# Kernel tuning notes

Hardware: AMD Instinct MI355X
Metric: run time of the kernel (lower is better)

Reference implementation:

```python
import jax, jax.numpy as jnp
import numpy as np

TEMP = 0.07
HARD_K = 512
EMB_D = 768
PROJ_D = 128
QUEUE = 32768
BATCH = 2048
NUM_CLASSES = 2


def setup_inputs() -> dict:
    key = jax.random.key(0)
    ks = jax.random.split(key, 8)
    embeddings = jax.random.normal(ks[0], (BATCH, EMB_D), dtype=jnp.float32)
    labels = jax.random.randint(ks[1], (BATCH,), 0, NUM_CLASSES)
    # projector params: Linear(D,D) -> ReLU -> Linear(D,128)
    W1 = jax.random.normal(ks[2], (EMB_D, EMB_D), dtype=jnp.float32) * 0.02
    b1 = jnp.zeros((EMB_D,), dtype=jnp.float32)
    W2 = jax.random.normal(ks[3], (EMB_D, PROJ_D), dtype=jnp.float32) * 0.02
    b2 = jnp.zeros((PROJ_D,), dtype=jnp.float32)
    # queue buffers: L2-normalized random embeddings (as in __init__) with valid labels
    qe = jax.random.normal(ks[4], (QUEUE, PROJ_D), dtype=jnp.float32)
    queue_embeddings = qe / jnp.linalg.norm(qe, axis=1, keepdims=True)
    queue_labels = jax.random.randint(ks[5], (QUEUE,), 0, NUM_CLASSES)
    return {
        'embeddings': embeddings, 'labels': labels,
        'W1': W1, 'b1': b1, 'W2': W2, 'b2': b2,
        'queue_embeddings': queue_embeddings, 'queue_labels': queue_labels,
    }


def reference(embeddings, labels, W1, b1, W2, b2, queue_embeddings, queue_labels):
    n = embeddings.shape[0]
    # projector + L2 normalize
    h = jax.nn.relu(embeddings @ W1 + b1)
    z = h @ W2 + b2
    z = z / jnp.linalg.norm(z, axis=1, keepdims=True)  # (N, 128)

    # pairwise in-batch similarities, scaled by temperature
    S = (z @ z.T) / TEMP  # (N, N)
    same = labels[:, None] == labels[None, :]
    eye = jnp.eye(n, dtype=bool)
    pos_mask = same & ~eye           # positives: same label, not self
    neg_mask = ~same                 # in-batch negatives: different label

    # logsumexp over in-batch negatives per anchor (-inf rows -> -inf, handled by logaddexp)
    neg_batch = jnp.where(neg_mask, S, -jnp.inf)
    lse_batch = jax.scipy.special.logsumexp(neg_batch, axis=1)  # (N,)

    # hard negatives from queue: opposite-label, top-K by similarity
    sims_q = z @ queue_embeddings.T  # (N, Q)
    opp = (queue_labels[None, :] != labels[:, None]) & (queue_labels[None, :] >= 0)
    masked_q = jnp.where(opp, sims_q, -jnp.inf)
    topk_vals, _ = jax.lax.top_k(masked_q, HARD_K)  # (N, K); -inf pads drop from logsumexp
    # fallback (no opposite-label entries): first K queue embeddings regardless of label
    fallback = sims_q[:, :HARD_K]
    has_opp = opp.any(axis=1, keepdims=True)
    neg_q = jnp.where(has_opp, topk_vals, fallback) / TEMP
    lse_queue = jax.scipy.special.logsumexp(neg_q, axis=1)  # (N,)

    # all negatives for anchor i: batch negatives ++ queue hard negatives
    lse_neg = jnp.logaddexp(lse_batch, lse_queue)  # (N,)

    # per positive pair (i, j): log_prob = pos_sim - logsumexp([pos_sim, negs])
    log_prob = S - jnp.logaddexp(S, lse_neg[:, None])  # (N, N)
    losses = jnp.where(pos_mask, -log_prob, 0.0)
    count = pos_mask.sum()
    return jnp.where(count > 0, losses.sum() / count.astype(losses.dtype), 0.0)
```

## Files before the change

kernel.cpp:

```cpp
#include <hip/hip_runtime.h>
#include <hip/hip_fp16.h>

#define BATCH_N   2048
#define EMB_D_    768
#define PROJ_D_   128
#define QUEUE_N   32768
#define HARD_K_   512
static constexpr float INV_T  = 1.0f / 0.07f;
static constexpr float WLO    = 0.12f;
static constexpr float S8ENC  = 255.0f / 0.88f;
static constexpr float BINW   = 0.88f / 255.0f;

typedef __attribute__((ext_vector_type(8))) short short8;
typedef __attribute__((ext_vector_type(4))) short short4v;
typedef __attribute__((ext_vector_type(4))) float f32x4;

__device__ __forceinline__ unsigned short f2bf(float f) {
    unsigned u = __float_as_uint(f);
    unsigned r = u + 0x7fffu + ((u >> 16) & 1u);
    return (unsigned short)(r >> 16);
}
__device__ __forceinline__ float bf2f(short s) {
    return __uint_as_float(((unsigned)(unsigned short)s) << 16);
}
__device__ __forceinline__ int opp_of(int mylab, const int* __restrict__ qcnt) {
    const int same = (mylab == 0) ? qcnt[0] : ((mylab == 1) ? qcnt[1] : 0);
    return qcnt[2] - same;
}

__global__ void __launch_bounds__(256) prep(const float* __restrict__ emb, short* __restrict__ embb,
                                            const float* __restrict__ queue, short* __restrict__ qb,
                                            const int* __restrict__ qlab, int* __restrict__ qpart,
                                            const float* __restrict__ W1, short* __restrict__ w1t,
                                            const float* __restrict__ W2, short* __restrict__ w2t,
                                            const int* __restrict__ labels, int* __restrict__ rcnt,
                                            int* __restrict__ pc) {
    __shared__ float tile[64][65];
    const int b = blockIdx.x, t = threadIdx.x;
    if (b < 1536) {
        const int i = b * 256 + t;
        const float4 f = ((const float4*)emb)[i];
        short4v o = {(short)f2bf(f.x), (short)f2bf(f.y), (short)f2bf(f.z), (short)f2bf(f.w)};
        ((short4v*)embb)[i] = o;
    } else if (b < 5632) {
        const int i = (b - 1536) * 256 + t;
        const float4 f = ((const float4*)queue)[i];
        short4v o = {(short)f2bf(f.x), (short)f2bf(f.y), (short)f2bf(f.z), (short)f2bf(f.w)};
        ((short4v*)qb)[i] = o;
    } else if (b < 5664) {
        const int i = (b - 5632) * 256 + t;
        int c0 = 0, c1 = 0, cv = 0;
        for (int j = i; j < QUEUE_N; j += 8192) {
            const int q = qlab[j];
            c0 += (q == 0); c1 += (q == 1); cv += (q >= 0);
        }
        #pragma unroll
        for (int o = 32; o > 0; o >>= 1) {
            c0 += __shfl_xor(c0, o); c1 += __shfl_xor(c1, o); cv += __shfl_xor(cv, o);
        }
        int* red = (int*)tile;
        const int wv = t >> 6;
        if ((t & 63) == 0) { red[wv * 4 + 0] = c0; red[wv * 4 + 1] = c1; red[wv * 4 + 2] = cv; }
        __syncthreads();
        if (t == 0) {
            const int bb = (b - 5632) * 4;
            qpart[bb + 0] = red[0] + red[4] + red[8]  + red[12];
            qpart[bb + 1] = red[1] + red[5] + red[9]  + red[13];
            qpart[bb + 2] = red[2] + red[6] + red[10] + red[14];
        }
    } else if (b < 5832) {
        const int bid = b - 5664;
        const float* A; short* At; int R, C, bx, by;
        if (bid < 144) { A = W1; At = w1t; R = EMB_D_; C = EMB_D_;  bx = (bid % 12) * 64; by = (bid / 12) * 64; }
        else { const int b2 = bid - 144; A = W2; At = w2t; R = EMB_D_; C = PROJ_D_; bx = (b2 & 1) * 64; by = (b2 >> 1) * 64; }
        const int tc = t & 63, tg = t >> 6;
        #pragma unroll
        for (int i = 0; i < 16; i++) {
            const int r = tg * 16 + i;
            tile[r][tc] = A[(size_t)(by + r) * C + bx + tc];
        }
        __syncthreads();
        #pragma unroll
        for (int i = 0; i < 16; i++) {
            const int r = tg * 16 + i;
            At[(size_t)(bx + r) * R + by + tc] = (short)f2bf(tile[tc][r]);
        }
    } else {
        int c = 0;
        for (int j = t; j < BATCH_N; j += 256) c += (labels[j] == 0);
        #pragma unroll
        for (int o = 32; o > 0; o >>= 1) c += __shfl_xor(c, o);
        int* red = (int*)tile;
        if ((t & 63) == 0) red[t >> 6] = c;
        __syncthreads();
        if (t == 0) rcnt[0] = red[0] + red[1] + red[2] + red[3];
        if (t < 8) pc[t] = 0;
    }
}

__global__ void __launch_bounds__(256) mfma_h64(const short* __restrict__ Ab,
                                                const short* __restrict__ Bb,
                                                const float* __restrict__ bias,
                                                short* __restrict__ C,
                                                int N, int K) {
    __shared__ __align__(16) short As[64 * 128];
    __shared__ __align__(16) short Bs[128 * 128];
    const int t = threadIdx.x;
    const int lane = t & 63, wv = t >> 6;
    const int l16 = lane & 15, l4 = lane >> 4;
    const int m0 = blockIdx.y * 64, n0 = blockIdx.x * 128;
    const int wn = wv * 32;

    f32x4 acc[4][2];
    #pragma unroll
    for (int i = 0; i < 4; ++i)
        #pragma unroll
        for (int j = 0; j < 2; ++j) acc[i][j] = f32x4{0.f, 0.f, 0.f, 0.f};

    for (int kb = 0; kb < K; kb += 128) {
        __syncthreads();
        #pragma unroll
        for (int it = 0; it < 4; ++it) {
            const int r = it * 4 + wv, row = r * 4 + l4, cg = l16 ^ (row & 15);
            __builtin_amdgcn_global_load_lds(
                (const __attribute__((address_space(1))) void*)(Ab + (size_t)(m0 + row) * K + kb + cg * 8),
                (__attribute__((address_space(3))) void*)(As + r * 512), 16, 0, 0);
        }
        #pragma unroll
        for (int it = 0; it < 8; ++it) {
            const int r = it * 4 + wv, row = r * 4 + l4, cg = l16 ^ (row & 15);
            __builtin_amdgcn_global_load_lds(
                (const __attribute__((address_space(1))) void*)(Bb + (size_t)(n0 + row) * K + kb + cg * 8),
                (__attribute__((address_space(3))) void*)(Bs + r * 512), 16, 0, 0);
        }
        __syncthreads();
        #pragma unroll
        for (int ks = 0; ks < 4; ++ks) {
            short8 af[4], bfr[2];
            const int ch = (ks * 4 + l4) ^ l16;
            #pragma unroll
            for (int i = 0; i < 4; ++i)
                af[i] = *(const short8*)(As + (i * 16 + l16) * 128 + ch * 8);
            #pragma unroll
            for (int j = 0; j < 2; ++j)
                bfr[j] = *(const short8*)(Bs + (wn + j * 16 + l16) * 128 + ch * 8);
            #pragma unroll
            for (int i = 0; i < 4; ++i)
                #pragma unroll
                for (int j = 0; j < 2; ++j)
                    acc[i][j] = __builtin_amdgcn_mfma_f32_16x16x32_bf16(af[i], bfr[j], acc[i][j], 0, 0, 0);
        }
    }

    float bsv[2];
    #pragma unroll
    for (int j = 0; j < 2; ++j) bsv[j] = bias[n0 + wn + j * 16 + l16];
    #pragma unroll
    for (int i = 0; i < 4; ++i)
        #pragma unroll
        for (int r = 0; r < 4; ++r) {
            const int m = m0 + i * 16 + l4 * 4 + r;
            #pragma unroll
            for (int j = 0; j < 2; ++j) {
                const int n = n0 + wn + j * 16 + l16;
                const float v = fmaxf(acc[i][j][r] + bsv[j], 0.0f);
                C[(size_t)m * N + n] = (short)f2bf(v);
            }
        }
}

__global__ void __launch_bounds__(256) znorm_perm(const short* __restrict__ Ab,
                                                  const short* __restrict__ Bb,
                                                  const float* __restrict__ bias,
                                                  short* __restrict__ zb,
                                                  const int* __restrict__ qlab,
                                                  const int* __restrict__ labels,
                                                  const int* __restrict__ qpart,
                                                  const int* __restrict__ rcnt,
                                                  int* __restrict__ qcnt,
                                                  int* __restrict__ colidx,
                                                  int* __restrict__ qlabp,
                                                  int* __restrict__ rowmap,
                                                  int* __restrict__ rlabp,
                                                  int* __restrict__ pc) {
    __shared__ __align__(16) short As[32 * 128];
    __shared__ __align__(16) short Bs[128 * 128];
    __shared__ float ssq[32];
    __shared__ int wcnt[4][3];
    __shared__ int gbase[3];
    const int blk = blockIdx.x;
    const int t = threadIdx.x;
    const int lane = t & 63, wv = t >> 6;

    if (blk >= 64) {
        const unsigned long long below = (1ull << lane) - 1ull;
        int q0 = 0, q1 = 0, qv = 0;
        for (int i = 0; i < 32; ++i) {
            q0 += qpart[i * 4]; q1 += qpart[i * 4 + 1]; qv += qpart[i * 4 + 2];
        }
        if (blk < 192) {
            const int cb = blk - 64;
            if (cb == 0 && t == 0) { qcnt[0] = q0; qcnt[1] = q1; qcnt[2] = qv; }
            const int j = cb * 256 + t;
            const int q = qlab[j];
            const int cls = (q == 0) ? 0 : ((q == 1) ? 1 : 2);
            const unsigned long long b0 = __ballot(cls == 0);
            const unsigned long long b1 = __ballot(cls == 1);
            const unsigned long long b2 = __ballot(cls == 2);
            const int rank = (cls == 0) ? __popcll(b0 & below)
                           : ((cls == 1) ? __popcll(b1 & below) : __popcll(b2 & below));
            if (lane == 0) {
                wcnt[wv][0] = __popcll(b0); wcnt[wv][1] = __popcll(b1); wcnt[wv][2] = __popcll(b2);
            }
            __syncthreads();
            if (t < 3) {
                const int tot = wcnt[0][t] + wcnt[1][t] + wcnt[2][t] + wcnt[3][t];
                gbase[t] = atomicAdd(&pc[t], tot);
            }
            __syncthreads();
            int wb = 0;
            #pragma unroll
            for (int w = 0; w < 4; ++w) if (w < wv) wb += wcnt[w][cls];
            const int cbase = (cls == 0) ? 0 : ((cls == 1) ? q0 : q0 + q1);
            const int pos = cbase + gbase[cls] + wb + rank;
            colidx[pos] = j; qlabp[pos] = q;
        } else {
            const int r = (blk - 192) * 256 + t;
            const int l = labels[r];
            const int cls = (l == 0) ? 0 : 1;
            const unsigned long long b0 = __ballot(cls == 0);
            const unsigned long long b1 = __ballot(cls == 1);
            const int rank = (cls == 0) ? __popcll(b0 & below) : __popcll(b1 & below);
            if (lane == 0) { wcnt[wv][0] = __popcll(b0); wcnt[wv][1] = __popcll(b1); }
            __syncthreads();
            if (t < 2) {
                const int tot = wcnt[0][t] + wcnt[1][t] + wcnt[2][t] + wcnt[3][t];
                gbase[t] = atomicAdd(&pc[3 + t], tot);
            }
            __syncthreads();
            int wb = 0;
            #pragma unroll
            for (int w = 0; w < 4; ++w) if (w < wv) wb += wcnt[w][cls];
            const int cbase = (cls == 0) ? 0 : rcnt[0];
            const int pos = cbase + gbase[cls] + wb + rank;
            rowmap[pos] = r; rlabp[pos] = l;
        }
        return;
    }

    const int l16 = lane & 15, l4 = lane >> 4;
    const int m0 = blk * 32;
    const int wn = wv * 32;
    const int K = EMB_D_;

    if (t < 32) ssq[t] = 0.0f;

    f32x4 acc[2][2];
    #pragma unroll
    for (int i = 0; i < 2; ++i)
        #pragma unroll
        for (int j = 0; j < 2; ++j) acc[i][j] = f32x4{0.f, 0.f, 0.f, 0.f};

    for (int kb = 0; kb < K; kb += 128) {
        __syncthreads();
        #pragma unroll
        for (int it = 0; it < 2; ++it) {
            const int r = it * 4 + wv, row = r * 4 + l4, cg = l16 ^ (row & 15);
            __builtin_amdgcn_global_load_lds(
                (const __attribute__((address_space(1))) void*)(Ab + (size_t)(m0 + row) * K + kb + cg * 8),
                (__attribute__((address_space(3))) void*)(As + r * 512), 16, 0, 0);
        }
        #pragma unroll
        for (int it = 0; it < 8; ++it) {
            const int r = it * 4 + wv, row = r * 4 + l4, cg = l16 ^ (row & 15);
            __builtin_amdgcn_global_load_lds(
                (const __attribute__((address_space(1))) void*)(Bb + (size_t)(row) * K + kb + cg * 8),
                (__attribute__((address_space(3))) void*)(Bs + r * 512), 16, 0, 0);
        }
        __syncthreads();
        #pragma unroll
        for (int ks = 0; ks < 4; ++ks) {
            short8 af[2], bfr[2];
            const int ch = (ks * 4 + l4) ^ l16;
            #pragma unroll
            for (int i = 0; i < 2; ++i)
                af[i] = *(const short8*)(As + (i * 16 + l16) * 128 + ch * 8);
            #pragma unroll
            for (int j = 0; j < 2; ++j)
                bfr[j] = *(const short8*)(Bs + (wn + j * 16 + l16) * 128 + ch * 8);
            #pragma unroll
            for (int i = 0; i < 2; ++i)
                #pragma unroll
                for (int j = 0; j < 2; ++j)
                    acc[i][j] = __builtin_amdgcn_mfma_f32_16x16x32_bf16(af[i], bfr[j], acc[i][j], 0, 0, 0);
        }
    }

    float bsv[2];
    #pragma unroll
    for (int j = 0; j < 2; ++j) bsv[j] = bias[wn + j * 16 + l16];
    #pragma unroll
    for (int i = 0; i < 2; ++i)
        #pragma unroll
        for (int r = 0; r < 4; ++r) {
            float p = 0.0f;
            #pragma unroll
            for (int j = 0; j < 2; ++j) {
                acc[i][j][r] += bsv[j];
                p += acc[i][j][r] * acc[i][j][r];
            }
            #pragma unroll
            for (int o = 8; o > 0; o >>= 1) p += __shfl_xor(p, o);
            if (l16 == 0) atomicAdd(&ssq[i * 16 + l4 * 4 + r], p);
        }
    __syncthreads();
    #pragma unroll
    for (int i = 0; i < 2; ++i)
        #pragma unroll
        for (int r = 0; r < 4; ++r) {
            const int lrow = i * 16 + l4 * 4 + r;
            const float inv = rsqrtf(ssq[lrow]);
            #pragma unroll
            for (int j = 0; j < 2; ++j)
                zb[(size_t)(m0 + lrow) * PROJ_D_ + wn + j * 16 + l16] =
                    (short)f2bf(acc[i][j][r] * inv);
        }
}

__global__ void __launch_bounds__(256) mfma_mask8(const short* __restrict__ Ab,
                                                  const short* __restrict__ Bb,
                                                  unsigned char* __restrict__ codes,
                                                  const int* __restrict__ rlabp,
                                                  const int* __restrict__ qlabp,
                                                  const int* __restrict__ colidx,
                                                  const int* __restrict__ rowmap,
                                                  const int* __restrict__ qcnt,
                                                  const int* __restrict__ rcnt) {
    const int m0 = blockIdx.y * 128;
    const int c0 = qcnt[0], c1v = qcnt[1], r0 = rcnt[0];
    int lo, hi;
    if (m0 + 128 <= r0)      { lo = c0; hi = c0 + c1v; }
    else if (m0 >= r0)       { lo = 0;  hi = c0; }
    else                     { lo = 0;  hi = c0 + c1v; }
    const int bs = blockIdx.x * 512;
    if (bs + 512 <= lo || bs >= hi) return;

    __shared__ __align__(16) short As[128 * 128];
    __shared__ __align__(16) short Bs[128 * 128];
    const int t = threadIdx.x;
    const int lane = t & 63, wv = t >> 6;
    const int l16 = lane & 15, l4 = lane >> 4;
    const int wm = (wv & 1) * 64, wn = (wv >> 1) * 64;

    int ra[8], ca[32], la[16], qa[16];
    #pragma unroll
    for (int it = 0; it < 8; ++it)
        ra[it] = rowmap[m0 + (it * 4 + wv) * 4 + l4];
    #pragma unroll
    for (int tt = 0; tt < 4; ++tt)
        #pragma unroll
        for (int it = 0; it < 8; ++it)
            ca[tt * 8 + it] = colidx[bs + tt * 128 + (it * 4 + wv) * 4 + l4];
    #pragma unroll
    for (int i = 0; i < 4; ++i)
        #pragma unroll
        for (int r = 0; r < 4; ++r)
            la[i * 4 + r] = rlabp[m0 + wm + i * 16 + l4 * 4 + r];
    #pragma unroll
    for (int tt = 0; tt < 4; ++tt)
        #pragma unroll
        for (int j = 0; j < 4; ++j)
            qa[tt * 4 + j] = qlabp[bs + tt * 128 + wn + j * 16 + l16];

    #pragma unroll
    for (int it = 0; it < 8; ++it) {
        const int r = it * 4 + wv, row = r * 4 + l4, cg = l16 ^ (row & 15);
        __builtin_amdgcn_global_load_lds(
            (const __attribute__((address_space(1))) void*)(Ab + (size_t)ra[it] * 128 + cg * 8),
            (__attribute__((address_space(3))) void*)(As + r * 512), 16, 0, 0);
    }
    #pragma unroll
    for (int it = 0; it < 8; ++it) {
        const int r = it * 4 + wv, row = r * 4 + l4, cg = l16 ^ (row & 15);
        __builtin_amdgcn_global_load_lds(
            (const __attribute__((address_space(1))) void*)(Bb + (size_t)ca[it] * 128 + cg * 8),
            (__attribute__((address_space(3))) void*)(Bs + r * 512), 16, 0, 0);
    }
    const float C0 = 1.0f - WLO * S8ENC;
    __syncthreads();

    #pragma unroll
    for (int tt = 0; tt < 4; ++tt) {
        const int n0 = bs + tt * 128;

        f32x4 acc[4][4];
        #pragma unroll
        for (int i = 0; i < 4; ++i)
            #pragma unroll
            for (int j = 0; j < 4; ++j) acc[i][j] = f32x4{0.f, 0.f, 0.f, 0.f};

        #pragma unroll
        for (int ks = 0; ks < 4; ++ks) {
            short8 af[4], bfr[4];
            const int ch = (ks * 4 + l4) ^ l16;
            #pragma unroll
            for (int i = 0; i < 4; ++i) {
                af[i]  = *(const short8*)(As + (wm + i * 16 + l16) * 128 + ch * 8);
                bfr[i] = *(const short8*)(Bs + (wn + i * 16 + l16) * 128 + ch * 8);
            }
            #pragma unroll
            for (int i = 0; i < 4; ++i)
                #pragma unroll
                for (int j = 0; j < 4; ++j)
                    acc[i][j] = __builtin_amdgcn_mfma_f32_16x16x32_bf16(af[i], bfr[j], acc[i][j], 0, 0, 0);
        }

        if (tt < 3) {
            __syncthreads();
            #pragma unroll
            for (int it = 0; it < 8; ++it) {
                const int r = it * 4 + wv, row = r * 4 + l4, cg = l16 ^ (row & 15);
                __builtin_amdgcn_global_load_lds(
                    (const __attribute__((address_space(1))) void*)(Bb + (size_t)ca[(tt + 1) * 8 + it] * 128 + cg * 8),
                    (__attribute__((address_space(3))) void*)(Bs + r * 512), 16, 0, 0);
            }
        }

        float a0[4], a1[4];
        #pragma unroll
        for (int j = 0; j < 4; ++j) {
            const int q = qa[tt * 4 + j];
            a0[j] = (q >= 0 && q != 0) ? C0 : -1e9f;
            a1[j] = (q >= 0 && q != 1) ? C0 : -1e9f;
        }
        #pragma unroll
        for (int i = 0; i < 4; ++i) {
            #pragma unroll
            for (int r = 0; r < 4; ++r) {
                const int m  = m0 + wm + i * 16 + l4 * 4 + r;
                const bool z = (la[i * 4 + r] == 0);
                unsigned pk = 0;
                #pragma unroll
                for (int j = 0; j < 4; ++j) {
                    const float add = z ? a0[j] : a1[j];
                    const float f = fmaf(acc[i][j][r], S8ENC, add);
#if __has_builtin(__builtin_amdgcn_cvt_pk_u8_f32)
                    pk = __builtin_amdgcn_cvt_pk_u8_f32(f, j, pk);
#else
                    const unsigned c = (unsigned)fminf(fmaxf(f, 0.0f), 255.0f);
                    pk |= c << (8 * j);
#endif
                }
                *(unsigned*)(codes + (size_t)m * QUEUE_N + n0 + wn + l16 * 4) = pk;
            }
        }
        if (tt < 3) __syncthreads();
    }
}

__device__ __forceinline__ void find_crossing(int* hist, int* grp, int target,
                                              int* s_bin, int* s_chi) {
    const int t = threadIdx.x;
    const int b0 = hist[4*t], b1 = hist[4*t+1], b2 = hist[4*t+2], b3 = hist[4*t+3];
    grp[t] = b0 + b1 + b2 + b3;
    __syncthreads();
    for (int off = 1; off < 256; off <<= 1) {
        int add = (t + off < 256) ? grp[t + off] : 0;
        __syncthreads();
        grp[t] += add;
        __syncthreads();
    }
    int cab = (t < 255) ? grp[t + 1] : 0;
    const int hb[4] = {b0, b1, b2, b3};
    #pragma unroll
    for (int i = 3; i >= 0; i--) {
        const int h = hb[i];
        if (cab < target && cab + h >= target) { *s_bin = 4*t + i; *s_chi = cab; }
        cab += h;
    }
    __syncthreads();
}

#define FOR_ALL_VALS(BODY)                                                   \
    _Pragma("unroll")                                                        \
    for (int _k = 0; _k < 64; _k++) {                                        \
        const float2 _f = __half22float2(*(const __half2*)&dv[_k]);          \
        { const float v = _f.x; BODY }                                       \
        { const float v = _f.y; BODY }                                       \
    }

__global__ void __launch_bounds__(256) tail_fused(const unsigned char* __restrict__ codes,
                                                  const int* __restrict__ qcnt,
                                                  const int* __restrict__ rlabp,
                                                  const int* __restrict__ rowmap,
                                                  const short* __restrict__ zb,
                                                  const short* __restrict__ qb,
                                                  const int* __restrict__ qlab,
                                                  float* __restrict__ lseq,
                                                  short* __restrict__ Sbuf) {
    __shared__ __align__(16) short As[128 * 128];
    __shared__ __align__(16) short Bs[128 * 128];
    __shared__ int s_bin, s_chi, s_bin2, s_chi2;
    __shared__ float scf[4];
    __shared__ int sci[4];
    const int bid = blockIdx.x, t = threadIdx.x;

    if (bid >= BATCH_N) {
        const int q = bid - BATCH_N;
        const int lane = t & 63, wv = t >> 6;
        const int l16 = lane & 15, l4 = lane >> 4;
        const int m0 = (q >> 4) * 128, n0 = (q & 15) * 128;

        #pragma unroll
        for (int it = 0; it < 8; ++it) {
            const int r = it * 4 + wv, row = r * 4 + l4, cg = l16 ^ (row & 15);
            __builtin_amdgcn_global_load_lds(
                (const __attribute__((address_space(1))) void*)(zb + (size_t)(m0 + row) * 128 + cg * 8),
                (__attribute__((address_space(3))) void*)(As + r * 512), 16, 0, 0);
        }
        #pragma unroll
        for (int it = 0; it < 8; ++it) {
            const int r = it * 4 + wv, row = r * 4 + l4, cg = l16 ^ (row & 15);
            __builtin_amdgcn_global_load_lds(
                (const __attribute__((address_space(1))) void*)(zb + (size_t)(n0 + row) * 128 + cg * 8),
                (__attribute__((address_space(3))) void*)(Bs + r * 512), 16, 0, 0);
        }
        __syncthreads();

        const int wm = (wv & 1) * 64, wn = (wv >> 1) * 64;
        f32x4 acc[4][4];
        #pragma unroll
        for (int i = 0; i < 4; ++i)
            #pragma unroll
            for (int j = 0; j < 4; ++j) acc[i][j] = f32x4{0.f, 0.f, 0.f, 0.f};

        #pragma unroll
        for (int ks = 0; ks < 4; ++ks) {
            short8 af[4], bfr[4];
            const int ch = (ks * 4 + l4) ^ l16;
            #pragma unroll
            for (int i = 0; i < 4; ++i) {
                af[i]  = *(const short8*)(As + (wm + i * 16 + l16) * 128 + ch * 8);
                bfr[i] = *(const short8*)(Bs + (wn + i * 16 + l16) * 128 + ch * 8);
            }
            #pragma unroll
            for (int i = 0; i < 4; ++i)
                #pragma unroll
                for (int j = 0; j < 4; ++j)
                    acc[i][j] = __builtin_amdgcn_mfma_f32_16x16x32_bf16(af[i], bfr[j], acc[i][j], 0, 0, 0);
        }
        #pragma unroll
        for (int i = 0; i < 4; ++i)
            #pragma unroll
            for (int r = 0; r < 4; ++r) {
                const int m = m0 + wm + i * 16 + l4 * 4 + r;
                union { unsigned short u[4]; uint2 d; } pk;
                #pragma unroll
                for (int j = 0; j < 4; ++j) pk.u[j] = f2bf(acc[i][j][r]);
                *(uint2*)(Sbuf + (size_t)m * BATCH_N + n0 + wn + l16 * 4) = pk.d;
            }
        return;
    }

    const int p = bid;
    const int orig  = rowmap[p];
    const int myLab = rlabp[p];
    const int opp   = opp_of(myLab, qcnt);
    bool fb = (opp < HARD_K_);
    if (!fb) {
        int* hist = (int*)Bs;
        int* suf  = (int*)(Bs + 512);
        hist[t] = 0;
        __syncthreads();

        const int c0 = qcnt[0];
        const int lo = (myLab == 0) ? c0 : 0;
        const int hi = (myLab == 0) ? c0 + qcnt[1] : c0;
        const int klo = (lo & ~511) >> 4;
        const int khi = ((hi + 511) & ~511) >> 4;

        const uint4* rowp = (const uint4*)(codes + (size_t)p * QUEUE_N);
        for (int k = klo + t; k < khi; k += 256) {
            const uint4 u = rowp[k];
            const unsigned w[4] = {u.x, u.y, u.z, u.w};
            #pragma unroll
            for (int q = 0; q < 4; q++)
                #pragma unroll
                for (int s = 0; s < 4; s++) {
                    const int c = (w[q] >> (8 * s)) & 0xFF;
                    if (c) atomicAdd(&hist[c], 1);
                }
        }
        __syncthreads();

        suf[t] = hist[t];
        __syncthreads();
        for (int off = 1; off < 256; off <<= 1) {
            int add = (t + off < 256) ? suf[t + off] : 0;
            __syncthreads();
            suf[t] += add;
            __syncthreads();
        }
        const int total = suf[1];
        if (total >= HARD_K_) {
            {
                const int above = (t < 255) ? suf[t + 1] : 0;
                if (suf[t] >= HARD_K_ && above < HARD_K_) s_bin = t;
            }
            __syncthreads();
            const int b = s_bin;

            float e = 0.0f;
            if (t > b && hist[t]) e = (float)hist[t] * __expf((WLO + ((float)t - 0.5f) * BINW - 1.0f) * INV_T);
            #pragma unroll
            for (int o = 32; o > 0; o >>= 1) e += __shfl_xor(e, o);
            if ((t & 63) == 0) scf[t >> 6] = e;
            __syncthreads();
            if (t == 0) {
                const float Eab  = scf[0] + scf[1] + scf[2] + scf[3];
                const int   cab  = (b < 255) ? suf[b + 1] : 0;
                const float ebin = __expf((WLO + ((float)b - 0.5f) * BINW - 1.0f) * INV_T);
                const float sadj = Eab + (float)(HARD_K_ - cab) * ebin;
                lseq[orig] = INV_T + __logf(sadj);
            }
            return;
        }
        __syncthreads();
    }

    float* zrow = (float*)As;
    int*   fh   = (int*)(As + 512);
    int*   grp  = (int*)(As + 2560);
    if (t < 128) zrow[t] = bf2f(zb[(size_t)orig * 128 + t]);
    __syncthreads();

    const int mylab = myLab;
    unsigned dv[64];
    float rm = -1e30f, rs = 0.0f;
    for (int k = 0; k < 128; k++) {
        const int j = t + 256 * k;
        float d = 0.0f;
        #pragma unroll
        for (int c = 0; c < 16; ++c) {
            const short8 qv = *(const short8*)(qb + (size_t)j * 128 + c * 8);
            #pragma unroll
            for (int e = 0; e < 8; ++e) d += zrow[c * 8 + e] * bf2f(qv[e]);
        }
        if (j < HARD_K_) {
            const float sv = d * INV_T;
            if (sv > rm) { rs = rs * __expf(rm - sv) + 1.0f; rm = sv; }
            else         { rs += __expf(sv - rm); }
        }
        const int q = qlab[j];
        const float mv = (q != mylab && q >= 0) ? d : -65504.0f;
        const __half h = __float2half(mv);
        unsigned short* pp = (unsigned short*)&dv[k >> 1];
        pp[k & 1] = *(const unsigned short*)&h;
    }

    if (opp == 0) {
        #pragma unroll
        for (int o = 32; o > 0; o >>= 1) {
            const float om = __shfl_xor(rm, o), os = __shfl_xor(rs, o);
            const float nm = fmaxf(rm, om);
            rs = rs * __expf(rm - nm) + os * __expf(om - nm);
            rm = nm;
        }
        if ((t & 63) == 0) { scf[t >> 6] = rm; ((float*)sci)[t >> 6] = rs; }
        __syncthreads();
        if (t == 0) {
            float M = -1e30f, Sx = 0.0f;
            for (int w = 0; w < 4; w++) {
                const float nm = fmaxf(M, scf[w]);
                Sx = Sx * __expf(M - nm) + ((float*)sci)[w] * __expf(scf[w] - nm);
                M = nm;
            }
            lseq[orig] = M + __logf(Sx);
        }
        return;
    }
    if (opp < HARD_K_) {
        float mm = -1e30f, ss = 0.0f;
        FOR_ALL_VALS(
            if (v > -60000.0f) {
                const float sv = v * INV_T;
                if (sv > mm) { ss = ss * __expf(mm - sv) + 1.0f; mm = sv; }
                else         { ss += __expf(sv - mm); }
            } )
        #pragma unroll
        for (int o = 32; o > 0; o >>= 1) {
            const float om = __shfl_xor(mm, o), os = __shfl_xor(ss, o);
            const float nm = fmaxf(mm, om);
            ss = ss * __expf(mm - nm) + os * __expf(om - nm);
            mm = nm;
        }
        if ((t & 63) == 0) { scf[t >> 6] = mm; ((float*)sci)[t >> 6] = ss; }
        __syncthreads();
        if (t == 0) {
            float M = -1e30f, Sx = 0.0f;
            for (int w = 0; w < 4; w++) {
                const float nm = fmaxf(M, scf[w]);
                Sx = Sx * __expf(M - nm) + ((float*)sci)[w] * __expf(scf[w] - nm);
                M = nm;
            }
            lseq[orig] = M + __logf(Sx);
        }
        return;
    }

    float mloc = -1e30f;
    FOR_ALL_VALS( mloc = fmaxf(mloc, v); )
    #pragma unroll
    for (int o = 32; o > 0; o >>= 1) mloc = fmaxf(mloc, __shfl_xor(mloc, o));
    if ((t & 63) == 0) scf[t >> 6] = mloc;
    __syncthreads();
    const float m = fmaxf(fmaxf(scf[0], scf[1]), fmaxf(scf[2], scf[3]));

    int c1 = 0, c2 = 0;
    const float w1 = m - 0.25f, w2 = m - 1.0f;
    FOR_ALL_VALS( c1 += (v >= w1); c2 += (v >= w2); )
    #pragma unroll
    for (int o = 32; o > 0; o >>= 1) { c1 += __shfl_xor(c1, o); c2 += __shfl_xor(c2, o); }
    if ((t & 63) == 0) { sci[t >> 6] = c1; }
    __syncthreads();
    const int C1 = sci[0] + sci[1] + sci[2] + sci[3];
    __syncthreads();
    if ((t & 63) == 0) { sci[t >> 6] = c2; }
    __syncthreads();
    const int C2 = sci[0] + sci[1] + sci[2] + sci[3];

    float lo;
    if      (C1 >= HARD_K_) lo = w1;
    else if (C2 >= HARD_K_) lo = w2;
    else                    lo = -1.01f;
    const float range = m - lo;
    const float scale = 1024.0f / range;

    for (int k = t; k < 1024; k += 256) fh[k] = 0;
    __syncthreads();
    FOR_ALL_VALS(
        if (v >= lo) {
            const float bf = fminf((v - lo) * scale, 1023.0f);
            atomicAdd(&fh[(int)bf], 1);
        } )
    __syncthreads();
    find_crossing(fh, grp, HARD_K_, &s_bin, &s_chi);
    const int   bin1 = s_bin, chi1 = s_chi;
    const float binw = range * (1.0f / 1024.0f);
    const float lo1  = lo + bin1 * binw;
    const float ssc  = 1024.0f / binw;

    for (int k = t; k < 1024; k += 256) fh[k] = 0;
    __syncthreads();
    FOR_ALL_VALS(
        if (v >= lo) {
            const float bf = fminf((v - lo) * scale, 1023.0f);
            if ((int)bf == bin1) {
                const float sf = fminf(fmaxf((v - lo1) * ssc, 0.0f), 1023.0f);
                atomicAdd(&fh[(int)sf], 1);
            }
        } )
    __syncthreads();
    find_crossing(fh, grp, HARD_K_ - chi1, &s_bin2, &s_chi2);
    const float thr = lo1 + s_bin2 * (binw * (1.0f / 1024.0f));

    float sl = 0.0f; int cg = 0;
    FOR_ALL_VALS( if (v > thr) { cg++; sl += __expf((v - m) * INV_T); } )
    #pragma unroll
    for (int o = 32; o > 0; o >>= 1) { sl += __shfl_xor(sl, o); cg += __shfl_xor(cg, o); }
    if ((t & 63) == 0) { scf[t >> 6] = sl; sci[t >> 6] = cg; }
    __syncthreads();
    if (t == 0) {
        const float slt = scf[0] + scf[1] + scf[2] + scf[3];
        const int   cgt = sci[0] + sci[1] + sci[2] + sci[3];
        const float sadj = slt + ((float)HARD_K_ - (float)cgt) * __expf((thr - m) * INV_T);
        lseq[orig] = m * INV_T + __logf(sadj);
    }
}

__global__ void __launch_bounds__(256) batch_row_loss(const short* __restrict__ S,
                                                      const int* __restrict__ labels,
                                                      const float* __restrict__ lse_queue,
                                                      float* __restrict__ part_out,
                                                      int* __restrict__ cnt_out) {
    const int t = threadIdx.x;
    const int wv = t >> 6, lane = t & 63;
    const int row = blockIdx.x * 4 + wv;
    __shared__ int plab[BATCH_N];
    for (int idx = t; idx < BATCH_N; idx += 256) {
        const int col = (idx & ~63) + ((idx & 3) << 4) + ((idx >> 2) & 15);
        plab[idx] = labels[col];
    }
    __syncthreads();
    const int myLab = labels[row];
    const uint4* rp = (const uint4*)(S + (size_t)row * BATCH_N);

    float v[32]; int lb[32];
    #pragma unroll
    for (int kk = 0; kk < 4; kk++) {
        const uint4 u = rp[lane + 64 * kk];
        const unsigned w[4] = {u.x, u.y, u.z, u.w};
        const int base = (lane + 64 * kk) * 8;
        #pragma unroll
        for (int q = 0; q < 4; q++) {
            v[kk * 8 + 2 * q]     = __uint_as_float(w[q] << 16);
            v[kk * 8 + 2 * q + 1] = __uint_as_float(w[q] & 0xFFFF0000u);
            lb[kk * 8 + 2 * q]     = plab[base + 2 * q];
            lb[kk * 8 + 2 * q + 1] = plab[base + 2 * q + 1];
        }
    }

    const float REF = INV_T;
    float sneg = 0.0f;
    #pragma unroll
    for (int k = 0; k < 32; k++) {
        const float ev = __expf(v[k] * INV_T - REF);
        sneg += (lb[k] != myLab) ? ev : 0.0f;
    }
    #pragma unroll
    for (int o = 32; o > 0; o >>= 1) sneg += __shfl_xor(sneg, o);
    const float lseb = (sneg > 0.0f) ? REF + __logf(sneg) : -1e30f;
    const float Lq = lse_queue[row];
    const float mx0 = fmaxf(lseb, Lq), mn0 = fminf(lseb, Lq);
    const float L = mx0 + __logf(1.0f + __expf(mn0 - mx0));

    float part = 0.0f; int cnt = 0;
    #pragma unroll
    for (int k = 0; k < 32; k++) {
        const int idx = ((lane + 64 * (k >> 3)) * 8) + (k & 7);
        const int col = (idx & ~63) + ((idx & 3) << 4) + ((idx >> 2) & 15);
        if (lb[k] == myLab && col != row) {
            const float sv = v[k] * INV_T;
            const float mx = fmaxf(sv, L), mn = fminf(sv, L);
            part += (mx - sv) + __logf(1.0f + __expf(mn - mx));
            cnt++;
        }
    }
    #pragma unroll
    for (int o = 32; o > 0; o >>= 1) { part += __shfl_xor(part, o); cnt += __shfl_xor(cnt, o); }
    if (lane == 0) { part_out[row] = part; cnt_out[row] = cnt; }
}

__global__ void __launch_bounds__(256) finalize_loss(const float* __restrict__ part,
                                                     const int* __restrict__ cnt,
                                                     float* __restrict__ out) {
    const int t = threadIdx.x;
    float s = 0.0f; int c = 0;
    #pragma unroll
    for (int k = 0; k < 8; k++) { s += part[t + 256 * k]; c += cnt[t + 256 * k]; }
    #pragma unroll
    for (int o = 32; o > 0; o >>= 1) { s += __shfl_xor(s, o); c += __shfl_xor(c, o); }
    __shared__ float sf[4]; __shared__ int sc[4];
    if ((t & 63) == 0) { sf[t >> 6] = s; sc[t >> 6] = c; }
    __syncthreads();
    if (t == 0) {
        const float st = sf[0] + sf[1] + sf[2] + sf[3];
        const int   ct = sc[0] + sc[1] + sc[2] + sc[3];
        out[0] = (ct > 0) ? (st / (float)ct) : 0.0f;
    }
}

extern "C" void kernel_launch(void* const* d_in, const int* in_sizes, int n_in,
                              void* d_out, int out_size, void* d_ws, size_t ws_size,
                              hipStream_t stream) {
    const float* emb    = (const float*)d_in[0];
    const int*   labels = (const int*)  d_in[1];
    const float* W1     = (const float*)d_in[2];
    const float* b1     = (const float*)d_in[3];
    const float* W2     = (const float*)d_in[4];
    const float* b2     = (const float*)d_in[5];
    const float* queue  = (const float*)d_in[6];
    const int*   qlab   = (const int*)  d_in[7];

    char* ws = (char*)d_ws;
    short*         Sbuf  = (short*)        (ws);
    unsigned char* codes = (unsigned char*)(ws + 16777216);
    short*         embb  = (short*)        (ws + 83886080);
    short*         hbf   = (short*)        (ws + 87031808);
    short*         zb    = (short*)        (ws + 90177536);
    short*         qb    = (short*)        (ws + 90701824);
    short*         w1t   = (short*)        (ws + 99090432);
    short*         w2t   = (short*)        (ws + 100270080);
    float*         lseq  = (float*)        (ws + 100466688);
    int*           qcnt  = (int*)          (ws + 100474880);
    int*           rcnt  = (int*)          (ws + 100474944);
    int*           pc    = (int*)          (ws + 100475008);
    int*           qpart = (int*)          (ws + 100475072);
    float*         partb = (float*)        (ws + 100475584);
    int*           cntb  = (int*)          (ws + 100483776);
    int*           colidx= (int*)          (ws + 100491968);
    int*           qlabp = (int*)          (ws + 100623040);
    int*           rowmap= (int*)          (ws + 100754112);
    int*           rlabp = (int*)          (ws + 100762304);

    dim3 blk(256);
    prep<<<dim3(5833), blk, 0, stream>>>(emb, embb, queue, qb, qlab, qpart, W1, w1t, W2, w2t, labels, rcnt, pc);
    mfma_h64<<<dim3(EMB_D_ / 128, BATCH_N / 64), blk, 0, stream>>>(embb, w1t, b1, hbf, EMB_D_, EMB_D_);
    znorm_perm<<<dim3(200), blk, 0, stream>>>(hbf, w2t, b2, zb, qlab, labels, qpart, rcnt,
                                              qcnt, colidx, qlabp, rowmap, rlabp, pc);
    mfma_mask8<<<dim3(QUEUE_N / 512, BATCH_N / 128), blk, 0, stream>>>(zb, qb, codes, rlabp, qlabp, colidx, rowmap, qcnt, rcnt);
    tail_fused<<<dim3(BATCH_N + 256), blk, 0, stream>>>(codes, qcnt, rlabp, rowmap, zb, qb, qlab, lseq, Sbuf);
    batch_row_loss<<<dim3(BATCH_N / 4), blk, 0, stream>>>(Sbuf, labels, lseq, partb, cntb);
    finalize_loss<<<1, blk, 0, stream>>>(partb, cntb, (float*)d_out);
}
```

Baseline: 192.6 us.

## Rebalance tiles, move S GEMM into mask kernel, fuse finalize, privatize histograms

The batch S=z·zᵀ GEMM moves out of the top-k tail kernel into the queue mask/GEMM kernel as extra blocks. Both GEMMs now use 64-row tiles, which doubles block count and cuts LDS use. The top-k kernel gets a smaller, dedicated LDS footprint with per-wave privatized histograms to reduce atomic contention. The finalize reduction is fused into the row-loss kernel with a last-block-done counter, dropping one launch. This adds risk: the done counter at pc+6 must be zeroed on every call, and the code shown does not make that visible.

```diff
diff --git a/kernel.cpp b/kernel.cpp
--- a/kernel.cpp
+++ b/kernel.cpp
@@ -327,34 +327,90 @@
         }
 }
 
-__global__ void __launch_bounds__(256) mfma_mask8(const short* __restrict__ Ab,
-                                                  const short* __restrict__ Bb,
-                                                  unsigned char* __restrict__ codes,
-                                                  const int* __restrict__ rlabp,
-                                                  const int* __restrict__ qlabp,
-                                                  const int* __restrict__ colidx,
-                                                  const int* __restrict__ rowmap,
-                                                  const int* __restrict__ qcnt,
-                                                  const int* __restrict__ rcnt) {
-    const int m0 = blockIdx.y * 128;
+__global__ void __launch_bounds__(256) mask8_spack(const short* __restrict__ zb,
+                                                   const short* __restrict__ qb,
+                                                   unsigned char* __restrict__ codes,
+                                                   const int* __restrict__ rlabp,
+                                                   const int* __restrict__ qlabp,
+                                                   const int* __restrict__ colidx,
+                                                   const int* __restrict__ rowmap,
+                                                   const int* __restrict__ qcnt,
+                                                   const int* __restrict__ rcnt,
+                                                   short* __restrict__ Sbuf) {
+    __shared__ __align__(16) short As[64 * 128];
+    __shared__ __align__(16) short Bs[128 * 128];
+    const int bid = blockIdx.x, t = threadIdx.x;
+    const int lane = t & 63, wv = t >> 6;
+    const int l16 = lane & 15, l4 = lane >> 4;
+    const int wm = (wv & 1) * 32, wn = (wv >> 1) * 64;
+
+    if (bid >= 2048) {
+        const int q = bid - 2048;
+        const int m0 = (q >> 4) * 64, n0 = (q & 15) * 128;
+        #pragma unroll
+        for (int it = 0; it < 4; ++it) {
+            const int r = it * 4 + wv, row = r * 4 + l4, cg = l16 ^ (row & 15);
+            __builtin_amdgcn_global_load_lds(
+                (const __attribute__((address_space(1))) void*)(zb + (size_t)(m0 + row) * 128 + cg * 8),
+                (__attribute__((address_space(3))) void*)(As + r * 512), 16, 0, 0);
+        }
+        #pragma unroll
+        for (int it = 0; it < 8; ++it) {
+            const int r = it * 4 + wv, row = r * 4 + l4, cg = l16 ^ (row & 15);
+            __builtin_amdgcn_global_load_lds(
+                (const __attribute__((address_space(1))) void*)(zb + (size_t)(n0 + row) * 128 + cg * 8),
+                (__attribute__((address_space(3))) void*)(Bs + r * 512), 16, 0, 0);
+        }
+        __syncthreads();
+
+        f32x4 acc[2][4];
+        #pragma unroll
+        for (int i = 0; i < 2; ++i)
+            #pragma unroll
+            for (int j = 0; j < 4; ++j) acc[i][j] = f32x4{0.f, 0.f, 0.f, 0.f};
+
+        #pragma unroll
+        for (int ks = 0; ks < 4; ++ks) {
+            short8 af[2], bfr[4];
+            const int ch = (ks * 4 + l4) ^ l16;
+            #pragma unroll
+            for (int i = 0; i < 2; ++i)
+                af[i]  = *(const short8*)(As + (wm + i * 16 + l16) * 128 + ch * 8);
+            #pragma unroll
+            for (int j = 0; j < 4; ++j)
+                bfr[j] = *(const short8*)(Bs + (wn + j * 16 + l16) * 128 + ch * 8);
+            #pragma unroll
+            for (int i = 0; i < 2; ++i)
+                #pragma unroll
+                for (int j = 0; j < 4; ++j)
+                    acc[i][j] = __builtin_amdgcn_mfma_f32_16x16x32_bf16(af[i], bfr[j], acc[i][j], 0, 0, 0);
+        }
+        #pragma unroll
+        for (int i = 0; i < 2; ++i)
+            #pragma unroll
+            for (int r = 0; r < 4; ++r) {
+                const int m = m0 + wm + i * 16 + l4 * 4 + r;
+                union { unsigned short u[4]; uint2 d; } pk;
+                #pragma unroll
+                for (int j = 0; j < 4; ++j) pk.u[j] = f2bf(acc[i][j][r]);
+                *(uint2*)(Sbuf + (size_t)m * BATCH_N + n0 + wn + l16 * 4) = pk.d;
+            }
+        return;
+    }
+
+    const int bx = bid & 63, by = bid >> 6;
+    const int m0 = by * 64;
     const int c0 = qcnt[0], c1v = qcnt[1], r0 = rcnt[0];
     int lo, hi;
-    if (m0 + 128 <= r0)      { lo = c0; hi = c0 + c1v; }
-    else if (m0 >= r0)       { lo = 0;  hi = c0; }
-    else                     { lo = 0;  hi = c0 + c1v; }
-    const int bs = blockIdx.x * 512;
+    if (m0 + 64 <= r0)  { lo = c0; hi = c0 + c1v; }
+    else if (m0 >= r0)  { lo = 0;  hi = c0; }
+    else                { lo = 0;  hi = c0 + c1v; }
+    const int bs = bx * 512;
     if (bs + 512 <= lo || bs >= hi) return;
 
-    __shared__ __align__(16) short As[128 * 128];
-    __shared__ __align__(16) short Bs[128 * 128];
-    const int t = threadIdx.x;
-    const int lane = t & 63, wv = t >> 6;
-    const int l16 = lane & 15, l4 = lane >> 4;
-    const int wm = (wv & 1) * 64, wn = (wv >> 1) * 64;
-
-    int ra[8], ca[32], la[16], qa[16];
-    #pragma unroll
-    for (int it = 0; it < 8; ++it)
+    int ra[4], ca[32], la[8], qa[16];
+    #pragma unroll
+    for (int it = 0; it < 4; ++it)
         ra[it] = rowmap[m0 + (it * 4 + wv) * 4 + l4];
     #pragma unroll
     for (int tt = 0; tt < 4; ++tt)
@@ -362,7 +418,7 @@
         for (int it = 0; it < 8; ++it)
             ca[tt * 8 + it] = colidx[bs + tt * 128 + (it * 4 + wv) * 4 + l4];
     #pragma unroll
-    for (int i = 0; i < 4; ++i)
+    for (int i = 0; i < 2; ++i)
         #pragma unroll
         for (int r = 0; r < 4; ++r)
             la[i * 4 + r] = rlabp[m0 + wm + i * 16 + l4 * 4 + r];
@@ -372,18 +428,18 @@
         for (int j = 0; j < 4; ++j)
             qa[tt * 4 + j] = qlabp[bs + tt * 128 + wn + j * 16 + l16];
 
+    #pragma unroll
+    for (int it = 0; it < 4; ++it) {
+        const int r = it * 4 + wv, row = r * 4 + l4, cg = l16 ^ (row & 15);
+        __builtin_amdgcn_global_load_lds(
+            (const __attribute__((address_space(1))) void*)(zb + (size_t)ra[it] * 128 + cg * 8),
+            (__attribute__((address_space(3))) void*)(As + r * 512), 16, 0, 0);
+    }
     #pragma unroll
     for (int it = 0; it < 8; ++it) {
         const int r = it * 4 + wv, row = r * 4 + l4, cg = l16 ^ (row & 15);
         __builtin_amdgcn_global_load_lds(
-            (const __attribute__((address_space(1))) void*)(Ab + (size_t)ra[it] * 128 + cg * 8),
-            (__attribute__((address_space(3))) void*)(As + r * 512), 16, 0, 0);
-    }
-    #pragma unroll
-    for (int it = 0; it < 8; ++it) {
-        const int r = it * 4 + wv, row = r * 4 + l4, cg = l16 ^ (row & 15);
-        __builtin_amdgcn_global_load_lds(
-            (const __attribute__((address_space(1))) void*)(Bb + (size_t)ca[it] * 128 + cg * 8),
+            (const __attribute__((address_space(1))) void*)(qb + (size_t)ca[it] * 128 + cg * 8),
             (__attribute__((address_space(3))) void*)(Bs + r * 512), 16, 0, 0);
     }
     const float C0 = 1.0f - WLO * S8ENC;
@@ -393,23 +449,24 @@
     for (int tt = 0; tt < 4; ++tt) {
         const int n0 = bs + tt * 128;
 
-        f32x4 acc[4][4];
-        #pragma unroll
-        for (int i = 0; i < 4; ++i)
+        f32x4 acc[2][4];
+        #pragma unroll
+        for (int i = 0; i < 2; ++i)
             #pragma unroll
             for (int j = 0; j < 4; ++j) acc[i][j] = f32x4{0.f, 0.f, 0.f, 0.f};
 
         #pragma unroll
         for (int ks = 0; ks < 4; ++ks) {
-            short8 af[4], bfr[4];
+            short8 af[2], bfr[4];
             const int ch = (ks * 4 + l4) ^ l16;
             #pragma unroll
-            for (int i = 0; i < 4; ++i) {
+            for (int i = 0; i < 2; ++i)
                 af[i]  = *(const short8*)(As + (wm + i * 16 + l16) * 128 + ch * 8);
-                bfr[i] = *(const short8*)(Bs + (wn + i * 16 + l16) * 128 + ch * 8);
-            }
-            #pragma unroll
-            for (int i = 0; i < 4; ++i)
+            #pragma unroll
+            for (int j = 0; j < 4; ++j)
+                bfr[j] = *(const short8*)(Bs + (wn + j * 16 + l16) * 128 + ch * 8);
+            #pragma unroll
+            for (int i = 0; i < 2; ++i)
                 #pragma unroll
                 for (int j = 0; j < 4; ++j)
                     acc[i][j] = __builtin_amdgcn_mfma_f32_16x16x32_bf16(af[i], bfr[j], acc[i][j], 0, 0, 0);
@@ -421,7 +478,7 @@
             for (int it = 0; it < 8; ++it) {
                 const int r = it * 4 + wv, row = r * 4 + l4, cg = l16 ^ (row & 15);
                 __builtin_amdgcn_global_load_lds(
-                    (const __attribute__((address_space(1))) void*)(Bb + (size_t)ca[(tt + 1) * 8 + it] * 128 + cg * 8),
+                    (const __attribute__((address_space(1))) void*)(qb + (size_t)ca[(tt + 1) * 8 + it] * 128 + cg * 8),
                     (__attribute__((address_space(3))) void*)(Bs + r * 512), 16, 0, 0);
             }
         }
@@ -434,7 +491,7 @@
             a1[j] = (q >= 0 && q != 1) ? C0 : -1e9f;
         }
         #pragma unroll
-        for (int i = 0; i < 4; ++i) {
+        for (int i = 0; i < 2; ++i) {
             #pragma unroll
             for (int r = 0; r < 4; ++r) {
                 const int m  = m0 + wm + i * 16 + l4 * 4 + r;
@@ -489,88 +546,27 @@
         { const float v = _f.y; BODY }                                       \
     }
 
-__global__ void __launch_bounds__(256) tail_fused(const unsigned char* __restrict__ codes,
-                                                  const int* __restrict__ qcnt,
-                                                  const int* __restrict__ rlabp,
-                                                  const int* __restrict__ rowmap,
-                                                  const short* __restrict__ zb,
-                                                  const short* __restrict__ qb,
-                                                  const int* __restrict__ qlab,
-                                                  float* __restrict__ lseq,
-                                                  short* __restrict__ Sbuf) {
-    __shared__ __align__(16) short As[128 * 128];
-    __shared__ __align__(16) short Bs[128 * 128];
+__global__ void __launch_bounds__(256) topk_fb(const unsigned char* __restrict__ codes,
+                                               const int* __restrict__ qcnt,
+                                               const int* __restrict__ rlabp,
+                                               const int* __restrict__ rowmap,
+                                               const short* __restrict__ zb,
+                                               const short* __restrict__ qb,
+                                               const int* __restrict__ qlab,
+                                               float* __restrict__ lseq) {
+    __shared__ int hist4[1024];
+    __shared__ int grp[256];
+    __shared__ float zrow[128];
     __shared__ int s_bin, s_chi, s_bin2, s_chi2;
     __shared__ float scf[4];
     __shared__ int sci[4];
-    const int bid = blockIdx.x, t = threadIdx.x;
-
-    if (bid >= BATCH_N) {
-        const int q = bid - BATCH_N;
-        const int lane = t & 63, wv = t >> 6;
-        const int l16 = lane & 15, l4 = lane >> 4;
-        const int m0 = (q >> 4) * 128, n0 = (q & 15) * 128;
-
-        #pragma unroll
-        for (int it = 0; it < 8; ++it) {
-            const int r = it * 4 + wv, row = r * 4 + l4, cg = l16 ^ (row & 15);
-            __builtin_amdgcn_global_load_lds(
-                (const __attribute__((address_space(1))) void*)(zb + (size_t)(m0 + row) * 128 + cg * 8),
-                (__attribute__((address_space(3))) void*)(As + r * 512), 16, 0, 0);
-        }
-        #pragma unroll
-        for (int it = 0; it < 8; ++it) {
-            const int r = it * 4 + wv, row = r * 4 + l4, cg = l16 ^ (row & 15);
-            __builtin_amdgcn_global_load_lds(
-                (const __attribute__((address_space(1))) void*)(zb + (size_t)(n0 + row) * 128 + cg * 8),
-                (__attribute__((address_space(3))) void*)(Bs + r * 512), 16, 0, 0);
-        }
-        __syncthreads();
-
-        const int wm = (wv & 1) * 64, wn = (wv >> 1) * 64;
-        f32x4 acc[4][4];
-        #pragma unroll
-        for (int i = 0; i < 4; ++i)
-            #pragma unroll
-            for (int j = 0; j < 4; ++j) acc[i][j] = f32x4{0.f, 0.f, 0.f, 0.f};
-
-        #pragma unroll
-        for (int ks = 0; ks < 4; ++ks) {
-            short8 af[4], bfr[4];
-            const int ch = (ks * 4 + l4) ^ l16;
-            #pragma unroll
-            for (int i = 0; i < 4; ++i) {
-                af[i]  = *(const short8*)(As + (wm + i * 16 + l16) * 128 + ch * 8);
-                bfr[i] = *(const short8*)(Bs + (wn + i * 16 + l16) * 128 + ch * 8);
-            }
-            #pragma unroll
-            for (int i = 0; i < 4; ++i)
-                #pragma unroll
-                for (int j = 0; j < 4; ++j)
-                    acc[i][j] = __builtin_amdgcn_mfma_f32_16x16x32_bf16(af[i], bfr[j], acc[i][j], 0, 0, 0);
-        }
-        #pragma unroll
-        for (int i = 0; i < 4; ++i)
-            #pragma unroll
-            for (int r = 0; r < 4; ++r) {
-                const int m = m0 + wm + i * 16 + l4 * 4 + r;
-                union { unsigned short u[4]; uint2 d; } pk;
-                #pragma unroll
-                for (int j = 0; j < 4; ++j) pk.u[j] = f2bf(acc[i][j][r]);
-                *(uint2*)(Sbuf + (size_t)m * BATCH_N + n0 + wn + l16 * 4) = pk.d;
-            }
-        return;
-    }
-
-    const int p = bid;
+    const int p = blockIdx.x, t = threadIdx.x;
     const int orig  = rowmap[p];
     const int myLab = rlabp[p];
     const int opp   = opp_of(myLab, qcnt);
-    bool fb = (opp < HARD_K_);
-    if (!fb) {
-        int* hist = (int*)Bs;
-        int* suf  = (int*)(Bs + 512);
-        hist[t] = 0;
+
+    if (opp >= HARD_K_) {
+        for (int k = t; k < 1024; k += 256) hist4[k] = 0;
         __syncthreads();
 
         const int c0 = qcnt[0];
@@ -579,6 +575,7 @@
         const int klo = (lo & ~511) >> 4;
         const int khi = ((hi + 511) & ~511) >> 4;
 
+        int* myh = hist4 + (t >> 6) * 256;
         const uint4* rowp = (const uint4*)(codes + (size_t)p * QUEUE_N);
         for (int k = klo + t; k < khi; k += 256) {
             const uint4 u = rowp[k];
@@ -588,37 +585,37 @@
                 #pragma unroll
                 for (int s = 0; s < 4; s++) {
                     const int c = (w[q] >> (8 * s)) & 0xFF;
-                    if (c) atomicAdd(&hist[c], 1);
+                    if (c) atomicAdd(&myh[c], 1);
                 }
         }
         __syncthreads();
-
-        suf[t] = hist[t];
+        const int h = hist4[t] + hist4[256 + t] + hist4[512 + t] + hist4[768 + t];
+        grp[t] = h;
         __syncthreads();
         for (int off = 1; off < 256; off <<= 1) {
-            int add = (t + off < 256) ? suf[t + off] : 0;
+            int add = (t + off < 256) ? grp[t + off] : 0;
             __syncthreads();
-            suf[t] += add;
+            grp[t] += add;
             __syncthreads();
         }
-        const int total = suf[1];
+        const int total = grp[1];
         if (total >= HARD_K_) {
             {
-                const int above = (t < 255) ? suf[t + 1] : 0;
-                if (suf[t] >= HARD_K_ && above < HARD_K_) s_bin = t;
+                const int above = (t < 255) ? grp[t + 1] : 0;
+                if (grp[t] >= HARD_K_ && above < HARD_K_) s_bin = t;
             }
             __syncthreads();
             const int b = s_bin;
 
             float e = 0.0f;
-            if (t > b && hist[t]) e = (float)hist[t] * __expf((WLO + ((float)t - 0.5f) * BINW - 1.0f) * INV_T);
+            if (t > b && h) e = (float)h * __expf((WLO + ((float)t - 0.5f) * BINW - 1.0f) * INV_T);
             #pragma unroll
             for (int o = 32; o > 0; o >>= 1) e += __shfl_xor(e, o);
             if ((t & 63) == 0) scf[t >> 6] = e;
             __syncthreads();
             if (t == 0) {
                 const float Eab  = scf[0] + scf[1] + scf[2] + scf[3];
-                const int   cab  = (b < 255) ? suf[b + 1] : 0;
+                const int   cab  = (b < 255) ? grp[b + 1] : 0;
                 const float ebin = __expf((WLO + ((float)b - 0.5f) * BINW - 1.0f) * INV_T);
                 const float sadj = Eab + (float)(HARD_K_ - cab) * ebin;
                 lseq[orig] = INV_T + __logf(sadj);
@@ -628,9 +625,7 @@
         __syncthreads();
     }
 
-    float* zrow = (float*)As;
-    int*   fh   = (int*)(As + 512);
-    int*   grp  = (int*)(As + 2560);
+    int* fh = hist4;
     if (t < 128) zrow[t] = bf2f(zb[(size_t)orig * 128 + t]);
     __syncthreads();
 
@@ -778,15 +773,18 @@
     }
 }
 
-__global__ void __launch_bounds__(256) batch_row_loss(const short* __restrict__ S,
-                                                      const int* __restrict__ labels,
-                                                      const float* __restrict__ lse_queue,
-                                                      float* __restrict__ part_out,
-                                                      int* __restrict__ cnt_out) {
+__global__ void __launch_bounds__(256) brl_final(const short* __restrict__ S,
+                                                 const int* __restrict__ labels,
+                                                 const float* __restrict__ lse_queue,
+                                                 float* __restrict__ part_out,
+                                                 int* __restrict__ cnt_out,
+                                                 int* __restrict__ done,
+                                                 float* __restrict__ out) {
     const int t = threadIdx.x;
     const int wv = t >> 6, lane = t & 63;
     const int row = blockIdx.x * 4 + wv;
     __shared__ int plab[BATCH_N];
+    __shared__ int s_last;
     for (int idx = t; idx < BATCH_N; idx += 256) {
         const int col = (idx & ~63) + ((idx & 3) << 4) + ((idx >> 2) & 15);
         plab[idx] = labels[col];
@@ -838,16 +836,24 @@
     }
     #pragma unroll
     for (int o = 32; o > 0; o >>= 1) { part += __shfl_xor(part, o); cnt += __shfl_xor(cnt, o); }
-    if (lane == 0) { part_out[row] = part; cnt_out[row] = cnt; }
-}
-
-__global__ void __launch_bounds__(256) finalize_loss(const float* __restrict__ part,
-                                                     const int* __restrict__ cnt,
-                                                     float* __restrict__ out) {
-    const int t = threadIdx.x;
+    if (lane == 0) {
+        atomicExch(&part_out[row], part);
+        atomicExch(&cnt_out[row], cnt);
+        __threadfence();
+    }
+    __syncthreads();
+    if (t == 0) s_last = (atomicAdd(done, 1) == (int)gridDim.x - 1);
+    __syncthreads();
+    if (!s_last) return;
+
+    __threadfence();
     float s = 0.0f; int c = 0;
     #pragma unroll
-    for (int k = 0; k < 8; k++) { s += part[t + 256 * k]; c += cnt[t + 256 * k]; }
+    for (int k = 0; k < 8; k++) {
+        const int idx = t + 256 * k;
+        s += atomicAdd(&part_out[idx], 0.0f);
+        c += atomicAdd(&cnt_out[idx], 0);
+    }
     #pragma unroll
     for (int o = 32; o > 0; o >>= 1) { s += __shfl_xor(s, o); c += __shfl_xor(c, o); }
     __shared__ float sf[4]; __shared__ int sc[4];
@@ -898,8 +904,7 @@
     mfma_h64<<<dim3(EMB_D_ / 128, BATCH_N / 64), blk, 0, stream>>>(embb, w1t, b1, hbf, EMB_D_, EMB_D_);
     znorm_perm<<<dim3(200), blk, 0, stream>>>(hbf, w2t, b2, zb, qlab, labels, qpart, rcnt,
                                               qcnt, colidx, qlabp, rowmap, rlabp, pc);
-    mfma_mask8<<<dim3(QUEUE_N / 512, BATCH_N / 128), blk, 0, stream>>>(zb, qb, codes, rlabp, qlabp, colidx, rowmap, qcnt, rcnt);
-    tail_fused<<<dim3(BATCH_N + 256), blk, 0, stream>>>(codes, qcnt, rlabp, rowmap, zb, qb, qlab, lseq, Sbuf);
-    batch_row_loss<<<dim3(BATCH_N / 4), blk, 0, stream>>>(Sbuf, labels, lseq, partb, cntb);
-    finalize_loss<<<1, blk, 0, stream>>>(partb, cntb, (float*)d_out);
-}
+    mask8_spack<<<dim3(2560), blk, 0, stream>>>(zb, qb, codes, rlabp, qlabp, colidx, rowmap, qcnt, rcnt, Sbuf);
+    topk_fb<<<dim3(BATCH_N), blk, 0, stream>>>(codes, qcnt, rlabp, rowmap, zb, qb, qlab, lseq);
+    brl_final<<<dim3(BATCH_N / 4), blk, 0, stream>>>(Sbuf, labels, lseq, partb, cntb, pc + 6, (float*)d_out);
+}
```

Result: faster. 185.8 us (-3.6%).
